# Optimization experiments

Measured on AMD Instinct MI355X. Metric: run time of the kernel, lower is better.

## Reference

```python
import jax, jax.numpy as jnp
import numpy as np

TAU = 1.0
EXP_ORDER = 12
LN_ORDER = 16
CLAMP = 5.0
LN_EPS = 1e-30


def _exp_taylor(x, order):
    # Horner evaluation of sum_{k=0}^{order} x^k / k!
    r = jnp.ones_like(x)
    for k in range(order, 0, -1):
        r = 1.0 + x * r / k
    return r


def _ln_taylor(y, order):
    # Taylor series of ln(y) about 1: sum_{k=1}^{order} (-1)^{k+1} (y-1)^k / k (Horner)
    z = y - 1.0
    r = jnp.zeros_like(z)
    for k in range(order, 0, -1):
        r = 1.0 / k - z * r
    return z * r


def _eml(ex, ey):
    # eml(x, y) = exp(x) + ln(y), both via Taylor series ('taylor' backend).
    return _exp_taylor(ex, EXP_ORDER) + _ln_taylor(ey, LN_ORDER)


def _gumbel_softmax(key, logits_bt, tau):
    g = jax.random.gumbel(key, logits_bt.shape, dtype=logits_bt.dtype)
    return jax.nn.softmax((logits_bt + g) / tau, axis=-1)


def _forward(x, logits_list, key):
    B, n_vars = x.shape
    x_exp = x[:, None, :]  # [B, 1, V]
    prev = None
    for level, logits in enumerate(logits_list):
        T, n_nodes, n_choices, _ = logits.shape
        key, kL, kR = jax.random.split(key, 3)
        lb = jnp.broadcast_to(logits[None, ..., 0], (B, T, n_nodes, n_choices))
        rb = jnp.broadcast_to(logits[None, ..., 1], (B, T, n_nodes, n_choices))
        left_w = _gumbel_softmax(kL, lb, TAU)   # [B,T,nodes,choices]
        right_w = _gumbel_softmax(kR, rb, TAU)
        shape = (B, T, n_nodes)
        cands = [jnp.ones(shape, x.dtype)]
        for v in range(n_vars):
            cands.append(jnp.broadcast_to(x_exp[:, :, v:v + 1], shape))
        cl = list(cands)
        cr = list(cands)
        if level > 0:
            cl.append(prev[:, :, 0::2])
            cr.append(prev[:, :, 1::2])
        eml_x = jnp.sum(jnp.stack(cl, axis=-1) * left_w, axis=-1)
        eml_y = jnp.sum(jnp.stack(cr, axis=-1) * right_w, axis=-1)
        eml_x = jnp.clip(eml_x, -CLAMP, CLAMP)
        eml_y = jnp.clip(eml_y, LN_EPS, None)
        prev = _eml(eml_x, eml_y)  # [B, T, n_nodes]
    return prev[..., 0]  # [B, T]


def setup_inputs() -> dict:
    key = jax.random.key(0)
    ks = jax.random.split(key, 7)
    B, T, n_vars, depth = 2048, 128, 4, 6
    nodes = [2 ** (depth - 1 - l) for l in range(depth)]
    inp = {"x": jax.random.normal(ks[0], (B, n_vars), dtype=jnp.float32)}
    for l in range(depth):
        n_choices = 1 + n_vars + (0 if l == 0 else 1)
        inp[f"logits_l{l}"] = 0.1 * jax.random.normal(
            ks[l + 1], (T, nodes[l], n_choices, 2), dtype=jnp.float32)
    return inp


def reference(x, logits_l0, logits_l1, logits_l2, logits_l3, logits_l4, logits_l5):
    logits_list = [logits_l0, logits_l1, logits_l2, logits_l3, logits_l4, logits_l5]
    return _forward(x, logits_list, jax.random.key(42))
```

## Files before the change

kernel.cpp:

```cpp
#include <hip/hip_runtime.h>
#include <stdint.h>

#define BLOCK 128

struct KeySet {
  uint32_t L0[6], L1[6], R0[6], R1[6];
};

__host__ __device__ inline void tf2x32(uint32_t k0, uint32_t k1,
                                       uint32_t x0, uint32_t x1,
                                       uint32_t& o0, uint32_t& o1) {
  const uint32_t k2 = k0 ^ k1 ^ 0x1BD11BDAu;
  x0 += k0; x1 += k1;
#define TFR(r) { x0 += x1; x1 = (x1 << (r)) | (x1 >> (32 - (r))); x1 ^= x0; }
  TFR(13) TFR(15) TFR(26) TFR(6)
  x0 += k1; x1 += k2 + 1u;
  TFR(17) TFR(29) TFR(16) TFR(24)
  x0 += k2; x1 += k0 + 2u;
  TFR(13) TFR(15) TFR(26) TFR(6)
  x0 += k0; x1 += k1 + 3u;
  TFR(17) TFR(29) TFR(16) TFR(24)
  x0 += k1; x1 += k2 + 4u;
  TFR(13) TFR(15) TFR(26) TFR(6)
  x0 += k2; x1 += k0 + 5u;
#undef TFR
  o0 = x0; o1 = x1;
}

__device__ __forceinline__ uint32_t rbits(uint32_t k0, uint32_t k1, uint32_t idx) {
  uint32_t o0, o1;
  tf2x32(k0, k1, 0u, idx, o0, o1);
  return o0 ^ o1;
}

__device__ __forceinline__ float log2_n(float x) { return __builtin_amdgcn_logf(x); }
__device__ __forceinline__ float exp2_n(float x) { return __builtin_amdgcn_exp2f(x); }

__device__ __forceinline__ float negg(uint32_t bits) {
  const float tiny = 1.17549435e-38f;
  float f = __uint_as_float((bits >> 9) | 0x3f800000u) - 1.0f;
  float u = fmaxf(f, tiny);
  return log2_n(-log2_n(u));
}

__device__ __forceinline__ float expT(float x) {
  float r = 2.0876756987868099e-9f;
  r = fmaf(r, x, 2.5052108385441719e-8f);
  r = fmaf(r, x, 2.7557319223985893e-7f);
  r = fmaf(r, x, 2.7557319223985888e-6f);
  r = fmaf(r, x, 2.4801587301587302e-5f);
  r = fmaf(r, x, 1.9841269841269841e-4f);
  r = fmaf(r, x, 1.3888888888888889e-3f);
  r = fmaf(r, x, 8.3333333333333332e-3f);
  r = fmaf(r, x, 4.1666666666666664e-2f);
  r = fmaf(r, x, 1.6666666666666666e-1f);
  r = fmaf(r, x, 0.5f);
  r = fmaf(r, x, 1.0f);
  r = fmaf(r, x, 1.0f);
  return r;
}

__device__ __forceinline__ float lnT(float y) {
  const float inv[16] = {1.0f/16.0f, 1.0f/15.0f, 1.0f/14.0f, 1.0f/13.0f, 1.0f/12.0f,
                         1.0f/11.0f, 0.1f, 1.0f/9.0f, 0.125f, 1.0f/7.0f, 1.0f/6.0f,
                         0.2f, 0.25f, 1.0f/3.0f, 0.5f, 1.0f};
  float z = y - 1.0f;
  float r = 0.0f;
#pragma unroll
  for (int i = 0; i < 16; ++i) r = fmaf(-z, r, inv[i]);
  return z * r;
}

template<int C>
__device__ __forceinline__ float smdot(const float* s, const float4& xv, float pc) {
  float m = s[0];
#pragma unroll
  for (int c = 1; c < C; ++c) m = fmaxf(m, s[c]);
  float e0 = exp2_n(s[0] - m), e1 = exp2_n(s[1] - m), e2 = exp2_n(s[2] - m),
        e3 = exp2_n(s[3] - m), e4 = exp2_n(s[4] - m);
  float den = e0 + e1 + e2 + e3 + e4;
  float num = fmaf(e4, xv.w, fmaf(e3, xv.z, fmaf(e2, xv.y, fmaf(e1, xv.x, e0))));
  if constexpr (C == 6) {
    float e5 = exp2_n(s[5] - m);
    den += e5;
    num = fmaf(e5, pc, num);
  }
  return num * __builtin_amdgcn_rcpf(den);
}

template<int C, bool HP>
__device__ __attribute__((noinline)) void level_body(
    int nodes, const float* __restrict__ lg,
    uint32_t kl0, uint32_t kl1, uint32_t kr0, uint32_t kr1,
    uint32_t base, float4 xv, float* __restrict__ pv) {
  for (int n = 0; n < nodes; ++n) {
    float sL[C], sR[C];
#pragma unroll
    for (int c = 0; c < C; ++c) {
      uint32_t idx = base + (uint32_t)(n * C + c);
      sL[c] = lg[(n * C + c) * 2]     - negg(rbits(kl0, kl1, idx));
      sR[c] = lg[(n * C + c) * 2 + 1] - negg(rbits(kr0, kr1, idx));
    }
    float pl = 0.0f, pr = 0.0f;
    if constexpr (HP) {
      pl = pv[(2 * n) * BLOCK];
      pr = pv[(2 * n + 1) * BLOCK];
    }
    float ex = smdot<C>(sL, xv, pl);
    float ey = smdot<C>(sR, xv, pr);
    ex = __builtin_amdgcn_fmed3f(ex, -5.0f, 5.0f);
    ey = fmaxf(ey, 1e-30f);
    pv[n * BLOCK] = expT(ex) + lnT(ey);
  }
}

__global__ __launch_bounds__(BLOCK, 4) void eml_kernel(
    const float* __restrict__ x,
    const float* __restrict__ g0, const float* __restrict__ g1,
    const float* __restrict__ g2, const float* __restrict__ g3,
    const float* __restrict__ g4, const float* __restrict__ g5,
    float* __restrict__ out, KeySet ks) {
  __shared__ float lgs[704];
  __shared__ float pvs[32 * BLOCK];
  const int tid = threadIdx.x;
  const int t = blockIdx.x & 127;
  const int chunk = blockIdx.x >> 7;

  const float LOG2E = 1.4426950408889634f;
  const float CADD  = 0.5287663729448977f;
  {
    const float* s0 = g0 + t * 320;
    for (int i = tid; i < 320; i += BLOCK) lgs[i] = fmaf(s0[i], LOG2E, CADD);
    const float* s1 = g1 + t * 192;
    for (int i = tid; i < 192; i += BLOCK) lgs[320 + i] = fmaf(s1[i], LOG2E, CADD);
    const float* s2 = g2 + t * 96;
    if (tid < 96) lgs[512 + tid] = fmaf(s2[tid], LOG2E, CADD);
    const float* s3 = g3 + t * 48;
    if (tid < 48) lgs[608 + tid] = fmaf(s3[tid], LOG2E, CADD);
    const float* s4 = g4 + t * 24;
    if (tid < 24) lgs[656 + tid] = fmaf(s4[tid], LOG2E, CADD);
    const float* s5 = g5 + t * 12;
    if (tid < 12) lgs[680 + tid] = fmaf(s5[tid], LOG2E, CADD);
  }
  __syncthreads();

  const int b = chunk * BLOCK + tid;
  const uint32_t bt = (uint32_t)(b * 128 + t);
  const float4 xv = reinterpret_cast<const float4*>(x)[b];
  float* pv = &pvs[tid];

  level_body<5, false>(32, lgs,       ks.L0[0], ks.L1[0], ks.R0[0], ks.R1[0], bt * 160u, xv, pv);
  level_body<6, true >(16, lgs + 320, ks.L0[1], ks.L1[1], ks.R0[1], ks.R1[1], bt * 96u,  xv, pv);
  level_body<6, true >( 8, lgs + 512, ks.L0[2], ks.L1[2], ks.R0[2], ks.R1[2], bt * 48u,  xv, pv);
  level_body<6, true >( 4, lgs + 608, ks.L0[3], ks.L1[3], ks.R0[3], ks.R1[3], bt * 24u,  xv, pv);
  level_body<6, true >( 2, lgs + 656, ks.L0[4], ks.L1[4], ks.R0[4], ks.R1[4], bt * 12u,  xv, pv);
  level_body<6, true >( 1, lgs + 680, ks.L0[5], ks.L1[5], ks.R0[5], ks.R1[5], bt * 6u,   xv, pv);

  out[bt] = pvs[tid];
}

extern "C" void kernel_launch(void* const* d_in, const int* in_sizes, int n_in,
                              void* d_out, int out_size, void* d_ws, size_t ws_size,
                              hipStream_t stream) {
  const float* x  = (const float*)d_in[0];
  const float* g0 = (const float*)d_in[1];
  const float* g1 = (const float*)d_in[2];
  const float* g2 = (const float*)d_in[3];
  const float* g3 = (const float*)d_in[4];
  const float* g4 = (const float*)d_in[5];
  const float* g5 = (const float*)d_in[6];
  float* out = (float*)d_out;

  KeySet ks;
  uint32_t K0 = 0u, K1 = 42u;
  for (int l = 0; l < 6; ++l) {
    uint32_t n0, n1, a0, a1, c0, c1;
    tf2x32(K0, K1, 0u, 0u, n0, n1);
    tf2x32(K0, K1, 0u, 1u, a0, a1);
    tf2x32(K0, K1, 0u, 2u, c0, c1);
    ks.L0[l] = a0; ks.L1[l] = a1;
    ks.R0[l] = c0; ks.R1[l] = c1;
    K0 = n0; K1 = n1;
  }

  eml_kernel<<<dim3(2048), dim3(BLOCK), 0, stream>>>(x, g0, g1, g2, g3, g4, g5, out, ks);
}
```

Before: 375.4 us.

## Replace Gumbel softmax exp/log with weight-times-reciprocal-log form and fold Threefry constants

Rewrites the Gumbel softmax algebraically. exp(l+g) becomes exp(l) * 1/(-ln u), so each candidate needs one log and one reciprocal instead of two logs and one exp2, and no max subtraction. Logit exponentials are precomputed per block into shared memory in an interleaved left/right layout, scaled by 2^-24 so the sum stays in range. Threefry key schedule constants are precomputed on the host, and the first key addition and final output adds are folded into the loop. Dropping the max-subtraction risks overflow or underflow if logits or uniforms are extreme, and the level function is now force-inlined instead of noinline.

```diff
diff --git a/kernel.cpp b/kernel.cpp
--- a/kernel.cpp
+++ b/kernel.cpp
@@ -4,12 +4,11 @@
 #define BLOCK 128
 
 struct KeySet {
-  uint32_t L0[6], L1[6], R0[6], R1[6];
+  uint32_t k0L[6], k1L[6], k2L[6], k0R[6], k1R[6], k2R[6];
 };
 
-__host__ __device__ inline void tf2x32(uint32_t k0, uint32_t k1,
-                                       uint32_t x0, uint32_t x1,
-                                       uint32_t& o0, uint32_t& o1) {
+__host__ inline void tf2x32(uint32_t k0, uint32_t k1, uint32_t x0, uint32_t x1,
+                            uint32_t& o0, uint32_t& o1) {
   const uint32_t k2 = k0 ^ k1 ^ 0x1BD11BDAu;
   x0 += k0; x1 += k1;
 #define TFR(r) { x0 += x1; x1 = (x1 << (r)) | (x1 >> (32 - (r))); x1 ^= x0; }
@@ -27,20 +26,33 @@
   o0 = x0; o1 = x1;
 }
 
-__device__ __forceinline__ uint32_t rbits(uint32_t k0, uint32_t k1, uint32_t idx) {
-  uint32_t o0, o1;
-  tf2x32(k0, k1, 0u, idx, o0, o1);
-  return o0 ^ o1;
-}
-
-__device__ __forceinline__ float log2_n(float x) { return __builtin_amdgcn_logf(x); }
-__device__ __forceinline__ float exp2_n(float x) { return __builtin_amdgcn_exp2f(x); }
-
-__device__ __forceinline__ float negg(uint32_t bits) {
+__device__ __forceinline__ uint32_t tf_fold(uint32_t k0, uint32_t k1, uint32_t k2,
+                                            uint32_t x1) {
+  uint32_t x0 = k0;
+#define R4(a,b,c,d) \
+  x0 += x1; x1 = __builtin_rotateleft32(x1,(a)); x1 ^= x0; \
+  x0 += x1; x1 = __builtin_rotateleft32(x1,(b)); x1 ^= x0; \
+  x0 += x1; x1 = __builtin_rotateleft32(x1,(c)); x1 ^= x0; \
+  x0 += x1; x1 = __builtin_rotateleft32(x1,(d)); x1 ^= x0;
+  R4(13,15,26,6)
+  x0 += k1; x1 += k2 + 1u;
+  R4(17,29,16,24)
+  x0 += k2; x1 += k0 + 2u;
+  R4(13,15,26,6)
+  x0 += k0; x1 += k1 + 3u;
+  R4(17,29,16,24)
+  x0 += k1; x1 += k2 + 4u;
+  R4(13,15,26,6)
+#undef R4
+  return (x0 + k2) ^ (x1 + (k0 + 5u));
+}
+
+__device__ __forceinline__ float wgt(uint32_t bits) {
   const float tiny = 1.17549435e-38f;
   float f = __uint_as_float((bits >> 9) | 0x3f800000u) - 1.0f;
   float u = fmaxf(f, tiny);
-  return log2_n(-log2_n(u));
+  float v = __builtin_amdgcn_logf(u);
+  return __builtin_amdgcn_rcpf(-v);
 }
 
 __device__ __forceinline__ float expT(float x) {
@@ -72,45 +84,53 @@
 }
 
 template<int C>
-__device__ __forceinline__ float smdot(const float* s, const float4& xv, float pc) {
-  float m = s[0];
-#pragma unroll
-  for (int c = 1; c < C; ++c) m = fmaxf(m, s[c]);
-  float e0 = exp2_n(s[0] - m), e1 = exp2_n(s[1] - m), e2 = exp2_n(s[2] - m),
-        e3 = exp2_n(s[3] - m), e4 = exp2_n(s[4] - m);
-  float den = e0 + e1 + e2 + e3 + e4;
-  float num = fmaf(e4, xv.w, fmaf(e3, xv.z, fmaf(e2, xv.y, fmaf(e1, xv.x, e0))));
+__device__ __forceinline__ float side_eval(const float* __restrict__ w8,
+    uint32_t k0, uint32_t k1, uint32_t k2, uint32_t x1b, float4 xv, float pc) {
+  float4 wa = *reinterpret_cast<const float4*>(w8);
+  float e  = wa.x * wgt(tf_fold(k0, k1, k2, x1b));
+  float den = e, num = e;
+  e = wa.y * wgt(tf_fold(k0, k1, k2, x1b + 1u)); den += e; num = fmaf(e, xv.x, num);
+  e = wa.z * wgt(tf_fold(k0, k1, k2, x1b + 2u)); den += e; num = fmaf(e, xv.y, num);
+  e = wa.w * wgt(tf_fold(k0, k1, k2, x1b + 3u)); den += e; num = fmaf(e, xv.z, num);
+  e = w8[4] * wgt(tf_fold(k0, k1, k2, x1b + 4u)); den += e; num = fmaf(e, xv.w, num);
   if constexpr (C == 6) {
-    float e5 = exp2_n(s[5] - m);
-    den += e5;
-    num = fmaf(e5, pc, num);
+    e = w8[5] * wgt(tf_fold(k0, k1, k2, x1b + 5u)); den += e; num = fmaf(e, pc, num);
   }
   return num * __builtin_amdgcn_rcpf(den);
 }
 
 template<int C, bool HP>
-__device__ __attribute__((noinline)) void level_body(
-    int nodes, const float* __restrict__ lg,
-    uint32_t kl0, uint32_t kl1, uint32_t kr0, uint32_t kr1,
-    uint32_t base, float4 xv, float* __restrict__ pv) {
+__device__ __forceinline__ void level_run(int nodes, const float* __restrict__ wl,
+    uint32_t k0L, uint32_t k1L, uint32_t k2L,
+    uint32_t k0R, uint32_t k1R, uint32_t k2R,
+    uint32_t bt, uint32_t stride, float4 xv, float* __restrict__ pv) {
+  const uint32_t xbL = bt * stride + k1L;
+  const uint32_t xbR = bt * stride + k1R;
   for (int n = 0; n < nodes; ++n) {
-    float sL[C], sR[C];
-#pragma unroll
-    for (int c = 0; c < C; ++c) {
-      uint32_t idx = base + (uint32_t)(n * C + c);
-      sL[c] = lg[(n * C + c) * 2]     - negg(rbits(kl0, kl1, idx));
-      sR[c] = lg[(n * C + c) * 2 + 1] - negg(rbits(kr0, kr1, idx));
-    }
     float pl = 0.0f, pr = 0.0f;
     if constexpr (HP) {
       pl = pv[(2 * n) * BLOCK];
       pr = pv[(2 * n + 1) * BLOCK];
     }
-    float ex = smdot<C>(sL, xv, pl);
-    float ey = smdot<C>(sR, xv, pr);
+    float ex = side_eval<C>(wl + n * 16,     k0L, k1L, k2L, xbL + (uint32_t)(n * C), xv, pl);
+    float ey = side_eval<C>(wl + n * 16 + 8, k0R, k1R, k2R, xbR + (uint32_t)(n * C), xv, pr);
     ex = __builtin_amdgcn_fmed3f(ex, -5.0f, 5.0f);
     ey = fmaxf(ey, 1e-30f);
     pv[n * BLOCK] = expT(ex) + lnT(ey);
+  }
+}
+
+template<int C>
+__device__ __forceinline__ void stage(const float* __restrict__ g, float* __restrict__ ws,
+                                      int t, int N, int woff, int tid) {
+  const int total = N * C * 2;
+  const float* src = g + t * total;
+  for (int i = tid; i < total; i += BLOCK) {
+    int n = i / (2 * C);
+    int rem = i - n * 2 * C;
+    int c = rem >> 1, s = rem & 1;
+    ws[woff + n * 16 + s * 8 + c] =
+        __builtin_amdgcn_exp2f(fmaf(src[i], 1.4426950408889634f, -24.0f));
   }
 }
 
@@ -120,28 +140,18 @@
     const float* __restrict__ g2, const float* __restrict__ g3,
     const float* __restrict__ g4, const float* __restrict__ g5,
     float* __restrict__ out, KeySet ks) {
-  __shared__ float lgs[704];
+  __shared__ float wz[1008];
   __shared__ float pvs[32 * BLOCK];
   const int tid = threadIdx.x;
   const int t = blockIdx.x & 127;
   const int chunk = blockIdx.x >> 7;
 
-  const float LOG2E = 1.4426950408889634f;
-  const float CADD  = 0.5287663729448977f;
-  {
-    const float* s0 = g0 + t * 320;
-    for (int i = tid; i < 320; i += BLOCK) lgs[i] = fmaf(s0[i], LOG2E, CADD);
-    const float* s1 = g1 + t * 192;
-    for (int i = tid; i < 192; i += BLOCK) lgs[320 + i] = fmaf(s1[i], LOG2E, CADD);
-    const float* s2 = g2 + t * 96;
-    if (tid < 96) lgs[512 + tid] = fmaf(s2[tid], LOG2E, CADD);
-    const float* s3 = g3 + t * 48;
-    if (tid < 48) lgs[608 + tid] = fmaf(s3[tid], LOG2E, CADD);
-    const float* s4 = g4 + t * 24;
-    if (tid < 24) lgs[656 + tid] = fmaf(s4[tid], LOG2E, CADD);
-    const float* s5 = g5 + t * 12;
-    if (tid < 12) lgs[680 + tid] = fmaf(s5[tid], LOG2E, CADD);
-  }
+  stage<5>(g0, wz, t, 32,   0, tid);
+  stage<6>(g1, wz, t, 16, 512, tid);
+  stage<6>(g2, wz, t,  8, 768, tid);
+  stage<6>(g3, wz, t,  4, 896, tid);
+  stage<6>(g4, wz, t,  2, 960, tid);
+  stage<6>(g5, wz, t,  1, 992, tid);
   __syncthreads();
 
   const int b = chunk * BLOCK + tid;
@@ -149,12 +159,18 @@
   const float4 xv = reinterpret_cast<const float4*>(x)[b];
   float* pv = &pvs[tid];
 
-  level_body<5, false>(32, lgs,       ks.L0[0], ks.L1[0], ks.R0[0], ks.R1[0], bt * 160u, xv, pv);
-  level_body<6, true >(16, lgs + 320, ks.L0[1], ks.L1[1], ks.R0[1], ks.R1[1], bt * 96u,  xv, pv);
-  level_body<6, true >( 8, lgs + 512, ks.L0[2], ks.L1[2], ks.R0[2], ks.R1[2], bt * 48u,  xv, pv);
-  level_body<6, true >( 4, lgs + 608, ks.L0[3], ks.L1[3], ks.R0[3], ks.R1[3], bt * 24u,  xv, pv);
-  level_body<6, true >( 2, lgs + 656, ks.L0[4], ks.L1[4], ks.R0[4], ks.R1[4], bt * 12u,  xv, pv);
-  level_body<6, true >( 1, lgs + 680, ks.L0[5], ks.L1[5], ks.R0[5], ks.R1[5], bt * 6u,   xv, pv);
+  level_run<5, false>(32, wz,       ks.k0L[0], ks.k1L[0], ks.k2L[0],
+                      ks.k0R[0], ks.k1R[0], ks.k2R[0], bt, 160u, xv, pv);
+  level_run<6, true >(16, wz + 512, ks.k0L[1], ks.k1L[1], ks.k2L[1],
+                      ks.k0R[1], ks.k1R[1], ks.k2R[1], bt,  96u, xv, pv);
+  level_run<6, true >( 8, wz + 768, ks.k0L[2], ks.k1L[2], ks.k2L[2],
+                      ks.k0R[2], ks.k1R[2], ks.k2R[2], bt,  48u, xv, pv);
+  level_run<6, true >( 4, wz + 896, ks.k0L[3], ks.k1L[3], ks.k2L[3],
+                      ks.k0R[3], ks.k1R[3], ks.k2R[3], bt,  24u, xv, pv);
+  level_run<6, true >( 2, wz + 960, ks.k0L[4], ks.k1L[4], ks.k2L[4],
+                      ks.k0R[4], ks.k1R[4], ks.k2R[4], bt,  12u, xv, pv);
+  level_run<6, true >( 1, wz + 992, ks.k0L[5], ks.k1L[5], ks.k2L[5],
+                      ks.k0R[5], ks.k1R[5], ks.k2R[5], bt,   6u, xv, pv);
 
   out[bt] = pvs[tid];
 }
@@ -178,8 +194,8 @@
     tf2x32(K0, K1, 0u, 0u, n0, n1);
     tf2x32(K0, K1, 0u, 1u, a0, a1);
     tf2x32(K0, K1, 0u, 2u, c0, c1);
-    ks.L0[l] = a0; ks.L1[l] = a1;
-    ks.R0[l] = c0; ks.R1[l] = c1;
+    ks.k0L[l] = a0; ks.k1L[l] = a1; ks.k2L[l] = a0 ^ a1 ^ 0x1BD11BDAu;
+    ks.k0R[l] = c0; ks.k1R[l] = c1; ks.k2R[l] = c0 ^ c1 ^ 0x1BD11BDAu;
     K0 = n0; K1 = n1;
   }
 
```

After: 350.3 us. -6.7%, faster.
